# Kernel optimization log

Measured on AMD Instinct MI355X. Metric: run time of the kernel, lower is better.

## Reference

```python
import jax, jax.numpy as jnp
import numpy as np

B, V, M, H = 256, 128, 256, 1024
TIMING_DIM = 10          # ceil(log2(max_timesteps=1024))
DECAY_ALPHA = 0.99
IN_DIM = (V + TIMING_DIM + 1 + 1) * M  # 35840


def setup_inputs() -> dict:
    key = jax.random.key(0)
    ks = jax.random.split(key, 12)
    x = jax.random.uniform(ks[0], (B, V), dtype=jnp.float32)
    memory = jax.random.uniform(ks[1], (B, M, V), dtype=jnp.float32)
    memory_timings = jax.random.randint(ks[2], (B, M), 0, 1000).astype(jnp.int64)
    memory_surprise = jax.random.uniform(ks[3], (B, M), dtype=jnp.float32)
    last_prediction = jax.random.uniform(ks[4], (B, V), dtype=jnp.float32)
    s1 = 1.0 / np.sqrt(IN_DIM)
    s2 = 1.0 / np.sqrt(H)
    W1 = jax.random.uniform(ks[5], (IN_DIM, H), dtype=jnp.float32, minval=-s1, maxval=s1)
    b1 = jnp.zeros((H,), jnp.float32)
    Wg = jax.random.uniform(ks[6], (IN_DIM, H), dtype=jnp.float32, minval=-s1, maxval=s1)
    bg = jnp.zeros((H,), jnp.float32)
    W2 = jax.random.uniform(ks[7], (H, V), dtype=jnp.float32, minval=-s2, maxval=s2)
    b2 = jnp.zeros((V,), jnp.float32)
    return {"x": x, "memory": memory, "memory_timings": memory_timings,
            "memory_surprise": memory_surprise, "last_prediction": last_prediction,
            "W1": W1, "b1": b1, "Wg": Wg, "bg": bg, "W2": W2, "b2": b2}


def _step(x, memory, memory_timings, memory_surprise, last_prediction):
    # surprise of incoming token under last prediction
    surprise = -jnp.log(jnp.sum(x * last_prediction, axis=1) + 1e-8)  # [B]
    # age + decay
    timings = memory_timings + 1
    surp = memory_surprise * DECAY_ALPHA
    # ring-buffer roll, write newest at slot 0
    mem = jnp.roll(memory, 1, axis=1).at[:, 0, :].set(x)
    timings = jnp.roll(timings, 1, axis=1).at[:, 0].set(0)
    surp = jnp.roll(surp, 1, axis=1).at[:, 0].set(surprise)
    # sort by age ascending, gather memory/surprise
    idx = jnp.argsort(timings, axis=1)                               # [B,M]
    sorted_timings = jnp.take_along_axis(timings, idx, axis=1)       # [B,M]
    sorted_memory = jnp.take_along_axis(mem, idx[..., None], axis=1)  # [B,M,V]
    sorted_surprise = jnp.take_along_axis(surp, idx, axis=1)          # [B,M]
    # binary encode timings
    powers = 2 ** jnp.arange(TIMING_DIM, dtype=sorted_timings.dtype)
    bits = ((sorted_timings[..., None] // powers) % 2).astype(jnp.float32)  # [B,M,T]
    norm_t = sorted_timings.astype(jnp.float32) / (
        jnp.max(sorted_timings, axis=1, keepdims=True).astype(jnp.float32) + 1.0)
    pred_input = jnp.concatenate(
        [sorted_memory.reshape(B, -1), bits.reshape(B, -1),
         norm_t.reshape(B, -1), sorted_surprise.reshape(B, -1)], axis=1)  # [B, IN_DIM]
    return pred_input


def reference(x, memory, memory_timings, memory_surprise, last_prediction,
              W1, b1, Wg, bg, W2, b2):
    pred_input = _step(x, memory, memory_timings, memory_surprise, last_prediction)
    # gated dense network: h = (xW1+b1) * sigmoid(xWg+bg); logits = hW2+b2
    h = (pred_input @ W1 + b1) * jax.nn.sigmoid(pred_input @ Wg + bg)
    return h @ W2 + b2
```

## Files before the change

kernel.cpp:

```cpp
#include <hip/hip_runtime.h>
#include <stdint.h>
#include <math.h>

#define BB 256
#define VV 128
#define MM 256
#define TDIM 10
#define HH 1024
#define IN_DIM 35840
#define KSPLIT 16
#define KSLICE 2240
#define BK 32
#define NCHUNK 70

using f32x4  = __attribute__((ext_vector_type(4))) float;
using bf16x8 = __attribute__((ext_vector_type(8))) short;

__device__ __forceinline__ unsigned short f2bf(float f) {
    unsigned int u = __float_as_uint(f);
    unsigned int r = (u + 0x7FFFu + ((u >> 16) & 1u)) >> 16;
    return (unsigned short)r;
}

__global__ __launch_bounds__(512)
void k_build(const float* __restrict__ x, const float* __restrict__ memory,
             const int* __restrict__ timings, const float* __restrict__ msurp,
             const float* __restrict__ lastp, short* __restrict__ A)
{
    int b = blockIdx.x, t = threadIdx.x;
    __shared__ int t_s[MM], idx_s[MM], st_s[MM];
    __shared__ float s_surprise;

    if (t < MM) t_s[t] = (t == 0) ? 0 : timings[b*MM + t - 1] + 1;
    if (t < 64) {
        float v = x[b*VV + t] * lastp[b*VV + t]
                + x[b*VV + t + 64] * lastp[b*VV + t + 64];
        #pragma unroll
        for (int off = 32; off > 0; off >>= 1)
            v += __shfl_down(v, off, 64);
        if (t == 0) s_surprise = -logf(v + 1e-8f);
    }
    __syncthreads();

    if (t < MM) {
        int ti = t_s[t], cnt = 0;
        #pragma unroll 4
        for (int j = 0; j < MM; ++j) {
            int tj = t_s[j];
            cnt += (tj < ti) || (tj == ti && j < t);
        }
        idx_s[cnt] = t;
        st_s[cnt]  = ti;
    }
    __syncthreads();

    short* Ab = A + (size_t)b * IN_DIM;
    if (t < MM) {
        float invm = 1.f / ((float)st_s[MM-1] + 1.f);
        int st = st_s[t], src = idx_s[t];
        #pragma unroll
        for (int tt = 0; tt < TDIM; ++tt)
            Ab[32768 + t*TDIM + tt] = (short)f2bf((float)((st >> tt) & 1));
        Ab[35328 + t] = (short)f2bf((float)st * invm);
        float sv = (src == 0) ? s_surprise : msurp[b*MM + src - 1] * 0.99f;
        Ab[35584 + t] = (short)f2bf(sv);
    }

    int q4 = t >> 7, v = t & (VV-1);
    float xv = x[b*VV + v];
    #pragma unroll 8
    for (int p = q4; p < MM; p += 4) {
        int src = idx_s[p];
        int row = (src == 0) ? 0 : src - 1;
        float mv = memory[((size_t)b*MM + row)*VV + v];
        float val = (src == 0) ? xv : mv;
        Ab[p*VV + v] = (short)f2bf(val);
    }
}

__global__ __launch_bounds__(512, 8)
void k_gemm(const short* __restrict__ A, const float* __restrict__ W1,
            const float* __restrict__ Wg, float* __restrict__ P)
{
    int ks = blockIdx.x;
    int xt = blockIdx.y;
    const float* W = (xt < 32) ? W1 : Wg;
    int wcol0 = (xt & 31) * 32;
    int pcol0 = xt * 32;
    int k0 = ks * KSLICE;

    __shared__ bf16x8 Ws8[2][128];

    int t = threadIdx.x;
    int l = t & 63, wv = t >> 6;
    int r = l & 15, q = l >> 4;

    const short* arow[2];
    #pragma unroll
    for (int mt = 0; mt < 2; ++mt) {
        int R = wv*32 + mt*16 + r;
        arow[mt] = A + (size_t)R*IN_DIM + k0 + q*8;
    }

    int boff[2];
    #pragma unroll
    for (int nt = 0; nt < 2; ++nt) {
        int R = nt*16 + r;
        boff[nt] = R*4 + (q ^ ((R >> 1) & 3));
    }

    f32x4 acc[2][2];
    #pragma unroll
    for (int mt = 0; mt < 2; ++mt)
        #pragma unroll
        for (int nt = 0; nt < 2; ++nt)
            acc[mt][nt] = (f32x4){0.f, 0.f, 0.f, 0.f};

    int wn  = t & 31;
    int wkb = (t >> 5) * 2;
    int wgr = wkb >> 3;
    int wslot16 = (wn*4 + (wgr ^ ((wn >> 1) & 3))) * 16 + (wkb & 7) * 2;
    const float* wbase = W + (size_t)(k0 + wkb)*HH + wcol0 + wn;

#define LOADA(AF, cc) do {                                                    \
        int ko_ = (cc)*BK;                                                    \
        _Pragma("unroll")                                                     \
        for (int mt_ = 0; mt_ < 2; ++mt_)                                     \
            AF[mt_] = *(const bf16x8*)(arow[mt_] + ko_);                      \
    } while (0)

#define WLOAD(wreg, cc) do {                                                  \
        const float* wp_ = wbase + (size_t)(cc)*BK*HH;                        \
        wreg[0] = wp_[0];                                                     \
        wreg[1] = wp_[HH];                                                    \
    } while (0)

#define WCONV(wreg, wdst) do {                                                \
        unsigned int dw_ = (unsigned int)f2bf(wreg[0])                        \
                         | ((unsigned int)f2bf(wreg[1]) << 16);               \
        *(unsigned int*)((char*)&Ws8[wdst][0] + wslot16) = dw_;               \
    } while (0)

    bf16x8 afA[2], afB[2];
    float wA[2], wB[2], w0[2];

    WLOAD(w0, 0);
    LOADA(afA, 0);
    WLOAD(wA, 1);
    WCONV(w0, 0);
    asm volatile("s_waitcnt lgkmcnt(0)" ::: "memory");
    __builtin_amdgcn_s_barrier();

#define CHUNK(c, AF, AFN, WCUR, WNXT) do {                                    \
        int cA_ = ((c) + 1 < NCHUNK) ? (c) + 1 : NCHUNK - 1;                  \
        int cW_ = ((c) + 2 < NCHUNK) ? (c) + 2 : NCHUNK - 1;                  \
        LOADA(AFN, cA_);                                                      \
        WLOAD(WNXT, cW_);                                                     \
        {                                                                     \
            bf16x8 bf_[2];                                                    \
            _Pragma("unroll")                                                 \
            for (int nt = 0; nt < 2; ++nt) bf_[nt] = Ws8[(c) & 1][boff[nt]];  \
            _Pragma("unroll")                                                 \
            for (int mt = 0; mt < 2; ++mt)                                    \
                _Pragma("unroll")                                             \
                for (int nt = 0; nt < 2; ++nt)                                \
                    acc[mt][nt] = __builtin_amdgcn_mfma_f32_16x16x32_bf16(    \
                        AF[mt], bf_[nt], acc[mt][nt], 0, 0, 0);               \
        }                                                                     \
        WCONV(WCUR, ((c) + 1) & 1);                                           \
        asm volatile("s_waitcnt lgkmcnt(0)" ::: "memory");                    \
        __builtin_amdgcn_s_barrier();                                         \
    } while (0)

    #pragma unroll 1
    for (int c = 0; c < NCHUNK; c += 2) {
        CHUNK(c,     afA, afB, wA, wB);
        CHUNK(c + 1, afB, afA, wB, wA);
    }
#undef CHUNK
#undef WCONV
#undef WLOAD
#undef LOADA

    #pragma unroll
    for (int mt = 0; mt < 2; ++mt)
        #pragma unroll
        for (int nt = 0; nt < 2; ++nt)
            #pragma unroll
            for (int rg = 0; rg < 4; ++rg) {
                int m = wv*32 + mt*16 + q*4 + rg;
                int n = pcol0 + nt*16 + r;
                P[((size_t)ks*BB + m)*2048 + n] = acc[mt][nt][rg];
            }
}

__global__ __launch_bounds__(512)
void k_tail(const float* __restrict__ P, const float* __restrict__ b1,
            const float* __restrict__ bg, const float* __restrict__ W2,
            const float* __restrict__ b2, float* __restrict__ out)
{
    int b = blockIdx.x, t = threadIdx.x;
    __shared__ f32x4 part[512];
    __shared__ float hs[HH];
    __shared__ float s2[512];

    const f32x4* P4 = (const f32x4*)P;
    f32x4 s = (f32x4){0.f, 0.f, 0.f, 0.f};
    #pragma unroll
    for (int ks = 0; ks < KSPLIT; ++ks)
        s += P4[((size_t)ks*BB + b)*512 + t];
    part[t] = s;
    __syncthreads();

    if (t < 256) {
        f32x4 p1 = part[t]       + ((const f32x4*)b1)[t];
        f32x4 pg = part[t + 256] + ((const f32x4*)bg)[t];
        f32x4 o;
        #pragma unroll
        for (int j = 0; j < 4; ++j)
            o[j] = p1[j] / (1.f + expf(-pg[j]));
        ((f32x4*)hs)[t] = o;
    }
    __syncthreads();

    int v = t & 127, kh = t >> 7;
    const float* wp = W2 + (size_t)kh*256*VV + v;
    const float* hk = hs + kh*256;
    float acc = 0.f;
    #pragma unroll 8
    for (int k = 0; k < 256; ++k)
        acc += hk[k] * wp[(size_t)k*VV];
    s2[t] = acc;
    __syncthreads();
    if (t < 128)
        out[(size_t)b*VV + v] = s2[t] + s2[t+128] + s2[t+256] + s2[t+384] + b2[v];
}

extern "C" void kernel_launch(void* const* d_in, const int* in_sizes, int n_in,
                              void* d_out, int out_size, void* d_ws, size_t ws_size,
                              hipStream_t stream)
{
    const float* x    = (const float*)d_in[0];
    const float* mem  = (const float*)d_in[1];
    const int*   tim  = (const int*)d_in[2];
    const float* msur = (const float*)d_in[3];
    const float* lp   = (const float*)d_in[4];
    const float* W1   = (const float*)d_in[5];
    const float* b1   = (const float*)d_in[6];
    const float* Wg   = (const float*)d_in[7];
    const float* bg   = (const float*)d_in[8];
    const float* W2   = (const float*)d_in[9];
    const float* b2   = (const float*)d_in[10];
    float* out = (float*)d_out;

    short* A = (short*)d_ws;
    float* P = (float*)((char*)d_ws + 18350080);

    k_build <<<256, 512, 0, stream>>>(x, mem, tim, msur, lp, A);
    k_gemm  <<<dim3(KSPLIT, 64), 512, 0, stream>>>(A, W1, Wg, P);
    k_tail  <<<256, 512, 0, stream>>>(P, b1, bg, W2, b2, out);
}
```

Before: 499.0 us.

## Fuse build, GEMM and tail into one cooperative kernel with larger GEMM tiles

Merges the three launches into a single cooperative kernel that uses grid-wide syncs between phases, with a fallback to three separate kernels. The GEMM is retiled to 256x128 output tiles per block (256 blocks instead of 1024). A is staged into LDS through global_load_lds and reused across 4 column waves, and W loads are widened to float2. The aim is to cut launch overhead and redundant A traffic, at the cost of grid-sync latency and fewer, heavier blocks that may leave CUs underused.

```diff
diff --git a/kernel.cpp b/kernel.cpp
--- a/kernel.cpp
+++ b/kernel.cpp
@@ -1,6 +1,9 @@
 #include <hip/hip_runtime.h>
+#include <hip/hip_cooperative_groups.h>
 #include <stdint.h>
 #include <math.h>
+
+namespace cg = cooperative_groups;
 
 #define BB 256
 #define VV 128
@@ -12,9 +15,13 @@
 #define KSLICE 2240
 #define BK 32
 #define NCHUNK 70
+#define BN 128
 
 using f32x4  = __attribute__((ext_vector_type(4))) float;
+using f32x2  = __attribute__((ext_vector_type(2))) float;
 using bf16x8 = __attribute__((ext_vector_type(8))) short;
+using u16x4  = __attribute__((ext_vector_type(4))) unsigned short;
+using u64x2  = __attribute__((ext_vector_type(2))) unsigned long long;
 
 __device__ __forceinline__ unsigned short f2bf(float f) {
     unsigned int u = __float_as_uint(f);
@@ -22,47 +29,70 @@
     return (unsigned short)r;
 }
 
-__global__ __launch_bounds__(512)
-void k_build(const float* __restrict__ x, const float* __restrict__ memory,
-             const int* __restrict__ timings, const float* __restrict__ msurp,
-             const float* __restrict__ lastp, short* __restrict__ A)
-{
-    int b = blockIdx.x, t = threadIdx.x;
-    __shared__ int t_s[MM], idx_s[MM], st_s[MM];
-    __shared__ float s_surprise;
-
-    if (t < MM) t_s[t] = (t == 0) ? 0 : timings[b*MM + t - 1] + 1;
+__device__ __forceinline__ void gload_lds16(const void* g, void* l) {
+    __builtin_amdgcn_global_load_lds(
+        (const __attribute__((address_space(1))) unsigned int*)g,
+        (__attribute__((address_space(3))) unsigned int*)l,
+        16, 0, 0);
+}
+
+struct SmemBuild {
+    int t_s[MM], idx_s[MM], st_s[MM];
+    float s_surprise;
+};
+struct SmemGemm {
+    bf16x8 As8[2][1024];
+    unsigned long long Wl[2][1024];
+};
+struct SmemTail {
+    f32x4 part[512];
+    float hs[HH];
+    float s2[512];
+};
+union SmemAll {
+    SmemBuild b;
+    SmemGemm  g;
+    SmemTail  t;
+};
+
+__device__ __forceinline__ void phase_build(
+    int b, int t, SmemBuild& sm,
+    const float* __restrict__ x, const float* __restrict__ memory,
+    const int* __restrict__ timings, const float* __restrict__ msurp,
+    const float* __restrict__ lastp, short* __restrict__ A)
+{
+    if (t < MM) sm.t_s[t] = (t == 0) ? 0 : timings[b*MM + t - 1] + 1;
     if (t < 64) {
         float v = x[b*VV + t] * lastp[b*VV + t]
                 + x[b*VV + t + 64] * lastp[b*VV + t + 64];
         #pragma unroll
         for (int off = 32; off > 0; off >>= 1)
             v += __shfl_down(v, off, 64);
-        if (t == 0) s_surprise = -logf(v + 1e-8f);
+        if (t == 0) sm.s_surprise = -logf(v + 1e-8f);
     }
     __syncthreads();
 
     if (t < MM) {
-        int ti = t_s[t], cnt = 0;
+        int ti = sm.t_s[t], cnt = 0;
         #pragma unroll 4
         for (int j = 0; j < MM; ++j) {
-            int tj = t_s[j];
+            int tj = sm.t_s[j];
             cnt += (tj < ti) || (tj == ti && j < t);
         }
-        idx_s[cnt] = t;
-        st_s[cnt]  = ti;
+        sm.idx_s[cnt] = t;
+        sm.st_s[cnt]  = ti;
     }
     __syncthreads();
 
     short* Ab = A + (size_t)b * IN_DIM;
     if (t < MM) {
-        float invm = 1.f / ((float)st_s[MM-1] + 1.f);
-        int st = st_s[t], src = idx_s[t];
+        float invm = 1.f / ((float)sm.st_s[MM-1] + 1.f);
+        int st = sm.st_s[t], src = sm.idx_s[t];
         #pragma unroll
         for (int tt = 0; tt < TDIM; ++tt)
             Ab[32768 + t*TDIM + tt] = (short)f2bf((float)((st >> tt) & 1));
         Ab[35328 + t] = (short)f2bf((float)st * invm);
-        float sv = (src == 0) ? s_surprise : msurp[b*MM + src - 1] * 0.99f;
+        float sv = (src == 0) ? sm.s_surprise : msurp[b*MM + src - 1] * 0.99f;
         Ab[35584 + t] = (short)f2bf(sv);
     }
 
@@ -70,7 +100,7 @@
     float xv = x[b*VV + v];
     #pragma unroll 8
     for (int p = q4; p < MM; p += 4) {
-        int src = idx_s[p];
+        int src = sm.idx_s[p];
         int row = (src == 0) ? 0 : src - 1;
         float mv = memory[((size_t)b*MM + row)*VV + v];
         float val = (src == 0) ? xv : mv;
@@ -78,162 +108,220 @@
     }
 }
 
-__global__ __launch_bounds__(512, 8)
-void k_gemm(const short* __restrict__ A, const float* __restrict__ W1,
-            const float* __restrict__ Wg, float* __restrict__ P)
-{
-    int ks = blockIdx.x;
-    int xt = blockIdx.y;
-    const float* W = (xt < 32) ? W1 : Wg;
-    int wcol0 = (xt & 31) * 32;
-    int pcol0 = xt * 32;
+__device__ __forceinline__ void phase_gemm(
+    int bid, int t, SmemGemm& sm,
+    const short* __restrict__ A, const float* __restrict__ W1,
+    const float* __restrict__ Wg, float* __restrict__ P)
+{
+    int ks = bid & 15, xt = bid >> 4;
+    const float* W = (xt < 8) ? W1 : Wg;
+    int wcol0 = (xt & 7) * BN;
+    int pcol0 = xt * BN;
     int k0 = ks * KSLICE;
 
-    __shared__ bf16x8 Ws8[2][128];
-
-    int t = threadIdx.x;
     int l = t & 63, wv = t >> 6;
     int r = l & 15, q = l >> 4;
-
-    const short* arow[2];
-    #pragma unroll
-    for (int mt = 0; mt < 2; ++mt) {
-        int R = wv*32 + mt*16 + r;
-        arow[mt] = A + (size_t)R*IN_DIM + k0 + q*8;
-    }
-
-    int boff[2];
+    int wm = wv >> 2, wn = wv & 3;
+
+    int aoff[8];
+    #pragma unroll
+    for (int mt = 0; mt < 8; ++mt) {
+        int R = wm*128 + mt*16 + r;
+        aoff[mt] = R*4 + (q ^ ((R >> 1) & 3));
+    }
+    int widx[2][2];
     #pragma unroll
     for (int nt = 0; nt < 2; ++nt) {
-        int R = nt*16 + r;
-        boff[nt] = R*4 + (q ^ ((R >> 1) & 3));
-    }
-
-    f32x4 acc[2][2];
-    #pragma unroll
-    for (int mt = 0; mt < 2; ++mt)
+        int n = wn*32 + nt*16 + r;
+        int s = (n >> 2) & 7;
+        widx[nt][0] = n*8 + ((2*q)     ^ s);
+        widx[nt][1] = n*8 + ((2*q + 1) ^ s);
+    }
+
+    f32x4 acc[8][2];
+    #pragma unroll
+    for (int mt = 0; mt < 8; ++mt)
         #pragma unroll
         for (int nt = 0; nt < 2; ++nt)
             acc[mt][nt] = (f32x4){0.f, 0.f, 0.f, 0.f};
 
-    int wn  = t & 31;
-    int wkb = (t >> 5) * 2;
-    int wgr = wkb >> 3;
-    int wslot16 = (wn*4 + (wgr ^ ((wn >> 1) & 3))) * 16 + (wkb & 7) * 2;
-    const float* wbase = W + (size_t)(k0 + wkb)*HH + wcol0 + wn;
-
-#define LOADA(AF, cc) do {                                                    \
-        int ko_ = (cc)*BK;                                                    \
+    const float* wbase = W + (size_t)(k0 + wv*4)*HH + wcol0 + l*2;
+    int wrow0 = l*2;
+    int wsA   = wv ^ ((l >> 1) & 7);
+
+#define STAGE_A(sbuf, cc) do {                                                \
+        int kc_ = k0 + (cc)*BK;                                               \
+        {   int G_ = t;                                                       \
+            int m_ = G_ >> 2;                                                 \
+            int kb_ = (G_ & 3) ^ ((m_ >> 1) & 3);                             \
+            gload_lds16(A + (size_t)m_*IN_DIM + kc_ + kb_*8,                  \
+                        (char*)&sm.As8[sbuf][0] + (size_t)(t & ~63)*16);      \
+        }                                                                     \
+        {   int G_ = t + 512;                                                 \
+            int m_ = G_ >> 2;                                                 \
+            int kb_ = (G_ & 3) ^ ((m_ >> 1) & 3);                             \
+            gload_lds16(A + (size_t)m_*IN_DIM + kc_ + kb_*8,                  \
+                        (char*)&sm.As8[sbuf][0] + (size_t)((t & ~63) + 512)*16);\
+        }                                                                     \
+    } while (0)
+
+#define WLOAD(wr, cc) do {                                                    \
+        const float* wp_ = wbase + (size_t)(cc)*BK*HH;                        \
         _Pragma("unroll")                                                     \
-        for (int mt_ = 0; mt_ < 2; ++mt_)                                     \
-            AF[mt_] = *(const bf16x8*)(arow[mt_] + ko_);                      \
+        for (int j_ = 0; j_ < 4; ++j_)                                        \
+            wr[j_] = *(const f32x2*)(wp_ + (size_t)j_*HH);                    \
     } while (0)
 
-#define WLOAD(wreg, cc) do {                                                  \
-        const float* wp_ = wbase + (size_t)(cc)*BK*HH;                        \
-        wreg[0] = wp_[0];                                                     \
-        wreg[1] = wp_[HH];                                                    \
+#define WCONV(wr, wdst) do {                                                  \
+        _Pragma("unroll")                                                     \
+        for (int i_ = 0; i_ < 2; ++i_) {                                      \
+            u16x4 pk_ = (u16x4){ f2bf(wr[0][i_]), f2bf(wr[1][i_]),            \
+                                 f2bf(wr[2][i_]), f2bf(wr[3][i_]) };          \
+            sm.Wl[wdst][(wrow0 + i_)*8 + wsA] =                               \
+                __builtin_bit_cast(unsigned long long, pk_);                  \
+        }                                                                     \
     } while (0)
 
-#define WCONV(wreg, wdst) do {                                                \
-        unsigned int dw_ = (unsigned int)f2bf(wreg[0])                        \
-                         | ((unsigned int)f2bf(wreg[1]) << 16);               \
-        *(unsigned int*)((char*)&Ws8[wdst][0] + wslot16) = dw_;               \
-    } while (0)
-
-    bf16x8 afA[2], afB[2];
-    float wA[2], wB[2], w0[2];
-
-    WLOAD(w0, 0);
-    LOADA(afA, 0);
+    f32x2 wA[4], wB[4];
+
+    STAGE_A(0, 0);
+    WLOAD(wB, 0);
+    STAGE_A(1, 1);
     WLOAD(wA, 1);
-    WCONV(w0, 0);
+    asm volatile("s_waitcnt vmcnt(6)" ::: "memory");
+    WCONV(wB, 0);
     asm volatile("s_waitcnt lgkmcnt(0)" ::: "memory");
     __builtin_amdgcn_s_barrier();
 
-#define CHUNK(c, AF, AFN, WCUR, WNXT) do {                                    \
+#define CHUNK(c, WCUR, WNXT) do {                                             \
         int cA_ = ((c) + 1 < NCHUNK) ? (c) + 1 : NCHUNK - 1;                  \
         int cW_ = ((c) + 2 < NCHUNK) ? (c) + 2 : NCHUNK - 1;                  \
-        LOADA(AFN, cA_);                                                      \
+        STAGE_A(((c) + 1) & 1, cA_);                                          \
         WLOAD(WNXT, cW_);                                                     \
+        asm volatile("s_waitcnt vmcnt(6)" ::: "memory");                      \
+        WCONV(WCUR, ((c) + 1) & 1);                                           \
         {                                                                     \
+            int pb_ = (c) & 1;                                                \
             bf16x8 bf_[2];                                                    \
             _Pragma("unroll")                                                 \
-            for (int nt = 0; nt < 2; ++nt) bf_[nt] = Ws8[(c) & 1][boff[nt]];  \
+            for (int nt = 0; nt < 2; ++nt) {                                  \
+                u64x2 wv2_;                                                   \
+                wv2_[0] = sm.Wl[pb_][widx[nt][0]];                            \
+                wv2_[1] = sm.Wl[pb_][widx[nt][1]];                            \
+                bf_[nt] = __builtin_bit_cast(bf16x8, wv2_);                   \
+            }                                                                 \
             _Pragma("unroll")                                                 \
-            for (int mt = 0; mt < 2; ++mt)                                    \
+            for (int mt = 0; mt < 8; ++mt) {                                  \
+                bf16x8 af_ = sm.As8[pb_][aoff[mt]];                           \
                 _Pragma("unroll")                                             \
                 for (int nt = 0; nt < 2; ++nt)                                \
                     acc[mt][nt] = __builtin_amdgcn_mfma_f32_16x16x32_bf16(    \
-                        AF[mt], bf_[nt], acc[mt][nt], 0, 0, 0);               \
+                        af_, bf_[nt], acc[mt][nt], 0, 0, 0);                  \
+            }                                                                 \
         }                                                                     \
-        WCONV(WCUR, ((c) + 1) & 1);                                           \
         asm volatile("s_waitcnt lgkmcnt(0)" ::: "memory");                    \
         __builtin_amdgcn_s_barrier();                                         \
     } while (0)
 
     #pragma unroll 1
     for (int c = 0; c < NCHUNK; c += 2) {
-        CHUNK(c,     afA, afB, wA, wB);
-        CHUNK(c + 1, afB, afA, wB, wA);
+        CHUNK(c,     wA, wB);
+        CHUNK(c + 1, wB, wA);
     }
 #undef CHUNK
 #undef WCONV
 #undef WLOAD
-#undef LOADA
-
-    #pragma unroll
-    for (int mt = 0; mt < 2; ++mt)
+#undef STAGE_A
+
+    #pragma unroll
+    for (int mt = 0; mt < 8; ++mt)
         #pragma unroll
         for (int nt = 0; nt < 2; ++nt)
             #pragma unroll
             for (int rg = 0; rg < 4; ++rg) {
-                int m = wv*32 + mt*16 + q*4 + rg;
-                int n = pcol0 + nt*16 + r;
+                int m = wm*128 + mt*16 + q*4 + rg;
+                int n = pcol0 + wn*32 + nt*16 + r;
                 P[((size_t)ks*BB + m)*2048 + n] = acc[mt][nt][rg];
             }
 }
 
-__global__ __launch_bounds__(512)
-void k_tail(const float* __restrict__ P, const float* __restrict__ b1,
-            const float* __restrict__ bg, const float* __restrict__ W2,
-            const float* __restrict__ b2, float* __restrict__ out)
-{
-    int b = blockIdx.x, t = threadIdx.x;
-    __shared__ f32x4 part[512];
-    __shared__ float hs[HH];
-    __shared__ float s2[512];
-
+__device__ __forceinline__ void phase_tail(
+    int b, int t, SmemTail& sm,
+    const float* __restrict__ P, const float* __restrict__ b1,
+    const float* __restrict__ bg, const float* __restrict__ W2,
+    const float* __restrict__ b2, float* __restrict__ out)
+{
     const f32x4* P4 = (const f32x4*)P;
     f32x4 s = (f32x4){0.f, 0.f, 0.f, 0.f};
     #pragma unroll
     for (int ks = 0; ks < KSPLIT; ++ks)
         s += P4[((size_t)ks*BB + b)*512 + t];
-    part[t] = s;
+    sm.part[t] = s;
     __syncthreads();
 
     if (t < 256) {
-        f32x4 p1 = part[t]       + ((const f32x4*)b1)[t];
-        f32x4 pg = part[t + 256] + ((const f32x4*)bg)[t];
+        f32x4 p1 = sm.part[t]       + ((const f32x4*)b1)[t];
+        f32x4 pg = sm.part[t + 256] + ((const f32x4*)bg)[t];
         f32x4 o;
         #pragma unroll
         for (int j = 0; j < 4; ++j)
             o[j] = p1[j] / (1.f + expf(-pg[j]));
-        ((f32x4*)hs)[t] = o;
+        ((f32x4*)sm.hs)[t] = o;
     }
     __syncthreads();
 
     int v = t & 127, kh = t >> 7;
     const float* wp = W2 + (size_t)kh*256*VV + v;
-    const float* hk = hs + kh*256;
+    const float* hk = sm.hs + kh*256;
     float acc = 0.f;
     #pragma unroll 8
     for (int k = 0; k < 256; ++k)
         acc += hk[k] * wp[(size_t)k*VV];
-    s2[t] = acc;
+    sm.s2[t] = acc;
     __syncthreads();
     if (t < 128)
-        out[(size_t)b*VV + v] = s2[t] + s2[t+128] + s2[t+256] + s2[t+384] + b2[v];
+        out[(size_t)b*VV + v] = sm.s2[t] + sm.s2[t+128] + sm.s2[t+256]
+                              + sm.s2[t+384] + b2[v];
+}
+
+__global__ __launch_bounds__(512, 2)
+void k_fused(const float* __restrict__ x, const float* __restrict__ mem,
+             const int* __restrict__ tim, const float* __restrict__ msur,
+             const float* __restrict__ lp, const float* __restrict__ W1,
+             const float* __restrict__ b1, const float* __restrict__ Wg,
+             const float* __restrict__ bg, const float* __restrict__ W2,
+             const float* __restrict__ b2, short* __restrict__ A,
+             float* __restrict__ P, float* __restrict__ out)
+{
+    __shared__ SmemAll sm;
+    int bid = blockIdx.x, t = threadIdx.x;
+
+    phase_build(bid, t, sm.b, x, mem, tim, msur, lp, A);
+    cg::this_grid().sync();
+    phase_gemm(bid, t, sm.g, A, W1, Wg, P);
+    cg::this_grid().sync();
+    phase_tail(bid, t, sm.t, P, b1, bg, W2, b2, out);
+}
+
+__global__ __launch_bounds__(512)
+void k_build_s(const float* x, const float* mem, const int* tim,
+               const float* msur, const float* lp, short* A)
+{
+    __shared__ SmemAll sm;
+    phase_build(blockIdx.x, threadIdx.x, sm.b, x, mem, tim, msur, lp, A);
+}
+__global__ __launch_bounds__(512, 2)
+void k_gemm_s(const short* A, const float* W1, const float* Wg, float* P)
+{
+    __shared__ SmemAll sm;
+    phase_gemm(blockIdx.x, threadIdx.x, sm.g, A, W1, Wg, P);
+}
+__global__ __launch_bounds__(512)
+void k_tail_s(const float* P, const float* b1, const float* bg,
+              const float* W2, const float* b2, float* out)
+{
+    __shared__ SmemAll sm;
+    phase_tail(blockIdx.x, threadIdx.x, sm.t, P, b1, bg, W2, b2, out);
 }
 
 extern "C" void kernel_launch(void* const* d_in, const int* in_sizes, int n_in,
@@ -256,7 +344,22 @@
     short* A = (short*)d_ws;
     float* P = (float*)((char*)d_ws + 18350080);
 
-    k_build <<<256, 512, 0, stream>>>(x, mem, tim, msur, lp, A);
-    k_gemm  <<<dim3(KSPLIT, 64), 512, 0, stream>>>(A, W1, Wg, P);
-    k_tail  <<<256, 512, 0, stream>>>(P, b1, bg, W2, b2, out);
-}
+    int coop = 0;
+    int dev = 0;
+    hipGetDevice(&dev);
+    hipDeviceGetAttribute(&coop, hipDeviceAttributeCooperativeLaunch, dev);
+
+    if (coop) {
+        void* kargs[] = { (void*)&x, (void*)&mem, (void*)&tim, (void*)&msur,
+                          (void*)&lp, (void*)&W1, (void*)&b1, (void*)&Wg,
+                          (void*)&bg, (void*)&W2, (void*)&b2, (void*)&A,
+                          (void*)&P,  (void*)&out };
+        hipError_t e = hipLaunchCooperativeKernel(
+            reinterpret_cast<void*>(k_fused), dim3(256), dim3(512),
+            kargs, 0, stream);
+        if (e == hipSuccess) return;
+    }
+    k_build_s<<<256, 512, 0, stream>>>(x, mem, tim, msur, lp, A);
+    k_gemm_s <<<256, 512, 0, stream>>>(A, W1, Wg, P);
+    k_tail_s <<<256, 512, 0, stream>>>(P, b1, bg, W2, b2, out);
+}
```

Result: faster. 479.8 us (-3.9%).
